# Performance work log

Hardware: AMD Instinct MI355X
Metric: run time of the kernel (lower is better)

Reference implementation:

```python
import jax, jax.numpy as jnp
import numpy as np

B, S, D, H = 2, 2048, 1024, 16
RANK = int(D * 0.2)  # 204, per decom(): rank = int(min(a,b)*ratio_LR)
HEAD = D // H


def setup_inputs() -> dict:
    key = jax.random.key(0)
    ks = jax.random.split(key, 16)
    s_in = 1.0 / np.sqrt(D)
    s_r = 1.0 / np.sqrt(RANK)
    inp = {
        'q': jax.random.normal(ks[0], (B, S, D), jnp.float32),
        'k': jax.random.normal(ks[1], (B, S, D), jnp.float32),
        'v': jax.random.normal(ks[2], (B, S, D), jnp.float32),
    }
    names = ['q', 'k', 'v', 'o']
    for i, n in enumerate(names):
        inp[f'V{n}'] = jax.random.uniform(ks[3 + 3 * i], (RANK, D), jnp.float32, -s_in, s_in)
        inp[f'U{n}'] = jax.random.uniform(ks[4 + 3 * i], (D, RANK), jnp.float32, -s_r, s_r)
        inp[f'b{n}'] = jax.random.uniform(ks[5 + 3 * i], (D,), jnp.float32, -s_r, s_r)
    return inp


def _factorized(x, Vw, Uw, b):
    # x @ V^T @ U^T + b  (low-rank linear: Linear(D->rank, no bias) then Linear(rank->D, bias))
    return jnp.einsum('bsr,dr->bsd', jnp.einsum('bsd,rd->bsr', x, Vw), Uw) + b


def _split_heads(x):
    # [B,S,D] -> [B,H,S,HEAD]
    return x.reshape(B, S, H, HEAD).transpose(0, 2, 1, 3)


def reference(q, k, v, Vq, Uq, bq, Vk, Uk, bk, Vv, Uv, bv, Vo, Uo, bo):
    qh = _split_heads(_factorized(q, Vq, Uq, bq))
    kh = _split_heads(_factorized(k, Vk, Uk, bk))
    vh = _split_heads(_factorized(v, Vv, Uv, bv))
    temperature = jnp.asarray(HEAD, jnp.float32) ** 0.5
    scores = jnp.einsum('bhqd,bhkd->bhqk', qh, kh) / temperature
    causal = jnp.tril(jnp.ones((S, S), bool))  # recreated each call in original
    scores = jnp.where(causal, scores, -jnp.inf)
    attn = jax.nn.softmax(scores, axis=-1)  # [B,H,S,S]
    out = jnp.einsum('bhqk,bhkd->bhqd', attn, vh)
    out = out.transpose(0, 2, 1, 3).reshape(B, S, D)
    out = _factorized(out, Vo, Uo, bo)
    # original returns attn flattened over batch*heads
    return out, attn.reshape(B * H, S, S)
```

## Files before the change

kernel.cpp:

```cpp
#include <hip/hip_runtime.h>
#include <stdint.h>

#define BB   2
#define SS   2048
#define DD   1024
#define NH   16
#define RK   204
#define RKP  256
#define HDIM 64
#define BH   (BB*NH)

typedef __attribute__((ext_vector_type(8))) short short8;
typedef __attribute__((ext_vector_type(4))) float f32x4;
typedef unsigned short u16;
typedef unsigned int   u32;

#define LOG2E  1.4426950408889634f

static __device__ __forceinline__ u32 cvtpk(float lo, float hi) {
    u32 r; asm("v_cvt_pk_bf16_f32 %0, %1, %2" : "=v"(r) : "v"(lo), "v"(hi)); return r;
}
static __device__ __forceinline__ u16 f2bf(float f) { return (u16)cvtpk(f, f); }
static __device__ __forceinline__ u32 pack2(float lo, float hi) { return cvtpk(lo, hi); }
static __device__ __forceinline__ float exp2_hw(float x) {
    float r; asm("v_exp_f32 %0, %1" : "=v"(r) : "v"(x)); return r;
}

struct C4 { const float *s0, *s1, *s2, *s3; u16 *d0, *d1, *d2, *d3; };

__global__ void cvt_bf16_b4(C4 c, int n4) {
    int y = blockIdx.y;
    const float* in = (y==0)?c.s0:(y==1)?c.s1:(y==2)?c.s2:c.s3;
    u16* out = (y==0)?c.d0:(y==1)?c.d1:(y==2)?c.d2:c.d3;
    int i = blockIdx.x * blockDim.x + threadIdx.x;
    if (i < n4) {
        float4 f = ((const float4*)in)[i];
        ((uint2*)out)[i] = make_uint2(pack2(f.x, f.y), pack2(f.z, f.w));
    }
}

__global__ void cvt_pad_b4(C4 c, int n) {
    int y = blockIdx.y;
    const float* in = (y==0)?c.s0:(y==1)?c.s1:(y==2)?c.s2:c.s3;
    u16* out = (y==0)?c.d0:(y==1)?c.d1:(y==2)?c.d2:c.d3;
    int i = blockIdx.x * blockDim.x + threadIdx.x;
    if (i >= n) return;
    int row = i >> 8, col = i & (RKP - 1);
    out[i] = (col < RK) ? f2bf(in[row * RK + col]) : (u16)0;
}

struct B3 {
    const void *A0, *A1, *A2;
    const u16  *B0, *B1, *B2;
    const float *bb0, *bb1, *bb2;
    void *C0, *C1, *C2;
};

#define LDW 136

template<int A_F32, int OUT_F32, int HAS_BIAS, int VT_LAST, int QSC>
__global__ __launch_bounds__(256)
void gemm_nt_k(B3 g, int lda, int ldb, int nrowsB, int ldc, int K)
{
    const int z = blockIdx.z;
    const void* Ap  = (z==0)?g.A0:(z==1)?g.A1:g.A2;
    const u16*  Bp  = (z==0)?g.B0:(z==1)?g.B1:g.B2;
    const float* bias = (z==0)?g.bb0:(z==1)?g.bb1:g.bb2;
    void* Cp = (z==0)?g.C0:(z==1)?g.C1:g.C2;

    __shared__ __align__(16) u16 As[64*LDW];
    __shared__ __align__(16) u16 Bs[64*LDW];
    const int row0 = blockIdx.x * 64;
    const int col0 = blockIdx.y * 64;
    const int t = threadIdx.x;
    const int w = t >> 6, lane = t & 63, quad = lane >> 4, l16 = lane & 15;
    const int r = t >> 2, seg = t & 3;

    f32x4 acc0 = 0.f, acc1 = 0.f, acc2 = 0.f, acc3 = 0.f;

    for (int k0 = 0; k0 < K; k0 += 128) {
        __syncthreads();
        if (A_F32) {
            const float* ga = (const float*)Ap + (size_t)(row0 + r) * lda + k0 + seg*32;
            float4 f0 = ((const float4*)ga)[0];
            float4 f1 = ((const float4*)ga)[1];
            float4 f2 = ((const float4*)ga)[2];
            float4 f3 = ((const float4*)ga)[3];
            float4 f4 = ((const float4*)ga)[4];
            float4 f5 = ((const float4*)ga)[5];
            float4 f6 = ((const float4*)ga)[6];
            float4 f7 = ((const float4*)ga)[7];
            uint4 s0 = { pack2(f0.x,f0.y), pack2(f0.z,f0.w), pack2(f1.x,f1.y), pack2(f1.z,f1.w) };
            uint4 s1 = { pack2(f2.x,f2.y), pack2(f2.z,f2.w), pack2(f3.x,f3.y), pack2(f3.z,f3.w) };
            uint4 s2 = { pack2(f4.x,f4.y), pack2(f4.z,f4.w), pack2(f5.x,f5.y), pack2(f5.z,f5.w) };
            uint4 s3 = { pack2(f6.x,f6.y), pack2(f6.z,f6.w), pack2(f7.x,f7.y), pack2(f7.z,f7.w) };
            *(uint4*)(As + r*LDW + seg*32)      = s0;
            *(uint4*)(As + r*LDW + seg*32 + 8)  = s1;
            *(uint4*)(As + r*LDW + seg*32 + 16) = s2;
            *(uint4*)(As + r*LDW + seg*32 + 24) = s3;
        } else {
            const u16* ga = (const u16*)Ap + (size_t)(row0 + r) * lda + k0 + seg*32;
            *(uint4*)(As + r*LDW + seg*32)      = ((const uint4*)ga)[0];
            *(uint4*)(As + r*LDW + seg*32 + 8)  = ((const uint4*)ga)[1];
            *(uint4*)(As + r*LDW + seg*32 + 16) = ((const uint4*)ga)[2];
            *(uint4*)(As + r*LDW + seg*32 + 24) = ((const uint4*)ga)[3];
        }
        {
            uint4 b0 = {0,0,0,0}, b1 = {0,0,0,0}, b2 = {0,0,0,0}, b3 = {0,0,0,0};
            if (col0 + r < nrowsB) {
                const u16* gb = Bp + (size_t)(col0 + r) * ldb + k0 + seg*32;
                b0 = ((const uint4*)gb)[0];
                b1 = ((const uint4*)gb)[1];
                b2 = ((const uint4*)gb)[2];
                b3 = ((const uint4*)gb)[3];
            }
            *(uint4*)(Bs + r*LDW + seg*32)      = b0;
            *(uint4*)(Bs + r*LDW + seg*32 + 8)  = b1;
            *(uint4*)(Bs + r*LDW + seg*32 + 16) = b2;
            *(uint4*)(Bs + r*LDW + seg*32 + 24) = b3;
        }
        __syncthreads();
        #pragma unroll
        for (int c = 0; c < 4; ++c) {
            short8 a = *(const short8*)(As + (w*16 + l16)*LDW + c*32 + quad*8);
            short8 b0v = *(const short8*)(Bs + (0*16 + l16)*LDW + c*32 + quad*8);
            acc0 = __builtin_amdgcn_mfma_f32_16x16x32_bf16(a, b0v, acc0, 0, 0, 0);
            short8 b1v = *(const short8*)(Bs + (1*16 + l16)*LDW + c*32 + quad*8);
            acc1 = __builtin_amdgcn_mfma_f32_16x16x32_bf16(a, b1v, acc1, 0, 0, 0);
            short8 b2v = *(const short8*)(Bs + (2*16 + l16)*LDW + c*32 + quad*8);
            acc2 = __builtin_amdgcn_mfma_f32_16x16x32_bf16(a, b2v, acc2, 0, 0, 0);
            short8 b3v = *(const short8*)(Bs + (3*16 + l16)*LDW + c*32 + quad*8);
            acc3 = __builtin_amdgcn_mfma_f32_16x16x32_bf16(a, b3v, acc3, 0, 0, 0);
        }
    }

    if (VT_LAST && z == 2) {
        __syncthreads();
        #pragma unroll
        for (int f = 0; f < 4; ++f) {
            f32x4 a = (f==0) ? acc0 : (f==1) ? acc1 : (f==2) ? acc2 : acc3;
            int col = f*16 + l16;
            float bv = HAS_BIAS ? bias[col0 + col] : 0.f;
            #pragma unroll
            for (int rg = 0; rg < 4; ++rg) {
                int rowl = w*16 + quad*4 + rg;
                As[col*72 + rowl] = f2bf(a[rg] + bv);
            }
        }
        __syncthreads();
        const int b_ = row0 >> 11;
        const int s0 = row0 & (SS - 1);
        const int h  = col0 >> 6;
        u16* dst = (u16*)Cp + ((size_t)((b_*NH + h)*HDIM + r))*SS + s0 + seg*16;
        ((uint4*)dst)[0] = *(const uint4*)(As + r*72 + seg*16);
        ((uint4*)dst)[1] = *(const uint4*)(As + r*72 + seg*16 + 8);
        return;
    }

    const float osc = (QSC && z == 0) ? 0.125f : 1.f;
    #pragma unroll
    for (int f = 0; f < 4; ++f) {
        f32x4 a = (f==0) ? acc0 : (f==1) ? acc1 : (f==2) ? acc2 : acc3;
        int col = col0 + f*16 + l16;
        float bv = HAS_BIAS ? bias[col] : 0.f;
        #pragma unroll
        for (int rg = 0; rg < 4; ++rg) {
            int rowg = row0 + w*16 + quad*4 + rg;
            float val = (a[rg] + bv) * osc;
            if (col >= nrowsB) val = 0.f;
            if (OUT_F32) ((float*)Cp)[(size_t)rowg*ldc + col] = val;
            else         ((u16*)Cp)[(size_t)rowg*ldc + col]  = f2bf(val);
        }
    }
}

#define QKT_8(BUF,sa0,sa1,sa2,sa3) do { \
    short8 b0 = *(const short8*)(BUF + (0*16 + l16)*72 + quad*8); \
    sa0 = __builtin_amdgcn_mfma_f32_16x16x32_bf16(q0, b0, sa0, 0,0,0); \
    short8 b0b = *(const short8*)(BUF + (0*16 + l16)*72 + 32 + quad*8); \
    sa0 = __builtin_amdgcn_mfma_f32_16x16x32_bf16(q1, b0b, sa0, 0,0,0); \
    short8 b1 = *(const short8*)(BUF + (1*16 + l16)*72 + quad*8); \
    sa1 = __builtin_amdgcn_mfma_f32_16x16x32_bf16(q0, b1, sa1, 0,0,0); \
    short8 b1b = *(const short8*)(BUF + (1*16 + l16)*72 + 32 + quad*8); \
    sa1 = __builtin_amdgcn_mfma_f32_16x16x32_bf16(q1, b1b, sa1, 0,0,0); \
    short8 b2 = *(const short8*)(BUF + (2*16 + l16)*72 + quad*8); \
    sa2 = __builtin_amdgcn_mfma_f32_16x16x32_bf16(q0, b2, sa2, 0,0,0); \
    short8 b2b = *(const short8*)(BUF + (2*16 + l16)*72 + 32 + quad*8); \
    sa2 = __builtin_amdgcn_mfma_f32_16x16x32_bf16(q1, b2b, sa2, 0,0,0); \
    short8 b3 = *(const short8*)(BUF + (3*16 + l16)*72 + quad*8); \
    sa3 = __builtin_amdgcn_mfma_f32_16x16x32_bf16(q0, b3, sa3, 0,0,0); \
    short8 b3b = *(const short8*)(BUF + (3*16 + l16)*72 + 32 + quad*8); \
    sa3 = __builtin_amdgcn_mfma_f32_16x16x32_bf16(q1, b3b, sa3, 0,0,0); \
} while (0)

static __device__ __forceinline__ void p1_int(
    const f32x4& sa0, const f32x4& sa1, const f32x4& sa2, const f32x4& sa3, float* l)
{
    #pragma unroll
    for (int rg = 0; rg < 4; ++rg) {
        l[rg] += (exp2_hw(sa0[rg]*LOG2E) + exp2_hw(sa1[rg]*LOG2E))
               + (exp2_hw(sa2[rg]*LOG2E) + exp2_hw(sa3[rg]*LOG2E));
    }
}
static __device__ __forceinline__ void p1_diag(
    const f32x4& sa0, const f32x4& sa1, const f32x4& sa2, const f32x4& sa3,
    float* l, int key0, int qg0)
{
    #pragma unroll
    for (int rg = 0; rg < 4; ++rg) {
        int qg = qg0 + rg;
        float e0 = (key0      <= qg) ? exp2_hw(sa0[rg]*LOG2E) : 0.f;
        float e1 = (key0 + 16 <= qg) ? exp2_hw(sa1[rg]*LOG2E) : 0.f;
        float e2 = (key0 + 32 <= qg) ? exp2_hw(sa2[rg]*LOG2E) : 0.f;
        float e3 = (key0 + 48 <= qg) ? exp2_hw(sa3[rg]*LOG2E) : 0.f;
        l[rg] += (e0+e1) + (e2+e3);
    }
}

__global__ __launch_bounds__(256)
void attn_k(const u16* __restrict__ qh, const u16* __restrict__ kh,
            const u16* __restrict__ vT,
            float* __restrict__ attn_out, u16* __restrict__ Ob)
{
    __shared__ __align__(16) u16 Ks[64*72];
    __shared__ __align__(16) u16 Vs[64*72];
    __shared__ __align__(16) u16 Ps[64*72];
    const int blk = blockIdx.x;
    const int qt = blk & 31, bh = blk >> 5;
    const int b_ = bh >> 4, h = bh & (NH - 1);
    const int qbase = qt * 64;
    const int t = threadIdx.x, w = t >> 6, lane = t & 63, quad = lane >> 4, l16 = lane & 15;
    const int r = t >> 2, seg = t & 3;

    const u16* qrow = qh + (size_t)(b_*SS + qbase + w*16 + l16)*DD + h*HDIM;
    short8 q0 = *(const short8*)(qrow + quad*8);
    short8 q1 = *(const short8*)(qrow + 32 + quad*8);

    const u16* kstage = kh + (size_t)(b_*SS + r)*DD + h*HDIM + seg*16;
    const u16* vstage = vT + ((size_t)(bh*HDIM + r))*SS + seg*16;
    const int qg0 = qbase + w*16 + quad*4;

    float l[4] = {0.f, 0.f, 0.f, 0.f};

    for (int kt0 = 0; kt0 <= qt; kt0 += 2) {
        const bool two = (kt0 + 1) <= qt;
        __syncthreads();
        {
            const u16* krow = kstage + (size_t)kt0*64*DD;
            *(uint4*)(Ks + r*72 + seg*16)     = ((const uint4*)krow)[0];
            *(uint4*)(Ks + r*72 + seg*16 + 8) = ((const uint4*)krow)[1];
            if (two) {
                const u16* krow2 = krow + (size_t)64*DD;
                *(uint4*)(Vs + r*72 + seg*16)     = ((const uint4*)krow2)[0];
                *(uint4*)(Vs + r*72 + seg*16 + 8) = ((const uint4*)krow2)[1];
            }
        }
        __syncthreads();
        {
            f32x4 sa0 = 0.f, sa1 = 0.f, sa2 = 0.f, sa3 = 0.f;
            QKT_8(Ks, sa0, sa1, sa2, sa3);
            if (kt0 < qt) p1_int(sa0, sa1, sa2, sa3, l);
            else          p1_diag(sa0, sa1, sa2, sa3, l, kt0*64 + l16, qg0);
        }
        if (two) {
            f32x4 sa0 = 0.f, sa1 = 0.f, sa2 = 0.f, sa3 = 0.f;
            QKT_8(Vs, sa0, sa1, sa2, sa3);
            if (kt0 + 1 < qt) p1_int(sa0, sa1, sa2, sa3, l);
            else              p1_diag(sa0, sa1, sa2, sa3, l, (kt0+1)*64 + l16, qg0);
        }
    }

    float lg2rl[4];
    #pragma unroll
    for (int rg = 0; rg < 4; ++rg) {
        #pragma unroll
        for (int d = 1; d < 16; d <<= 1) l[rg] += __shfl_xor(l[rg], d);
        lg2rl[rg] = -__log2f(l[rg]);
    }

    f32x4 oa0 = 0.f, oa1 = 0.f, oa2 = 0.f, oa3 = 0.f;
    float* attn_base = attn_out + (size_t)bh * SS * SS;
    float* rp0 = attn_base + (size_t)(qg0 + 0)*SS + l16;
    float* rp1 = attn_base + (size_t)(qg0 + 1)*SS + l16;
    float* rp2 = attn_base + (size_t)(qg0 + 2)*SS + l16;
    float* rp3 = attn_base + (size_t)(qg0 + 3)*SS + l16;
    const int psrow = w*16 + quad*4;

    for (int kt = 0; kt <= qt; ++kt) {
        __syncthreads();
        {
            const u16* krow = kstage + (size_t)kt*64*DD;
            *(uint4*)(Ks + r*72 + seg*16)     = ((const uint4*)krow)[0];
            *(uint4*)(Ks + r*72 + seg*16 + 8) = ((const uint4*)krow)[1];
            const u16* vrow = vstage + kt*64;
            *(uint4*)(Vs + r*72 + seg*16)     = ((const uint4*)vrow)[0];
            *(uint4*)(Vs + r*72 + seg*16 + 8) = ((const uint4*)vrow)[1];
        }
        __syncthreads();

        f32x4 sa0 = 0.f, sa1 = 0.f, sa2 = 0.f, sa3 = 0.f;
        QKT_8(Ks, sa0, sa1, sa2, sa3);

        if (kt < qt) {
            #pragma unroll
            for (int f = 0; f < 4; ++f) {
                f32x4 sv = (f==0) ? sa0 : (f==1) ? sa1 : (f==2) ? sa2 : sa3;
                float p0 = exp2_hw(__builtin_fmaf(sv[0], LOG2E, lg2rl[0]));
                float p1 = exp2_hw(__builtin_fmaf(sv[1], LOG2E, lg2rl[1]));
                float p2 = exp2_hw(__builtin_fmaf(sv[2], LOG2E, lg2rl[2]));
                float p3 = exp2_hw(__builtin_fmaf(sv[3], LOG2E, lg2rl[3]));
                rp0[f*16] = p0; rp1[f*16] = p1; rp2[f*16] = p2; rp3[f*16] = p3;
                u32 pk01 = cvtpk(p0, p1), pk23 = cvtpk(p2, p3);
                Ps[(psrow+0)*72 + f*16 + l16] = (u16)pk01;
                Ps[(psrow+1)*72 + f*16 + l16] = (u16)(pk01 >> 16);
                Ps[(psrow+2)*72 + f*16 + l16] = (u16)pk23;
                Ps[(psrow+3)*72 + f*16 + l16] = (u16)(pk23 >> 16);
            }
        } else {
            int kbase = kt*64;
            #pragma unroll
            for (int f = 0; f < 4; ++f) {
                f32x4 sv = (f==0) ? sa0 : (f==1) ? sa1 : (f==2) ? sa2 : sa3;
                int key = kbase + f*16 + l16;
                float p0 = (key <= qg0+0) ? exp2_hw(__builtin_fmaf(sv[0], LOG2E, lg2rl[0])) : 0.f;
                float p1 = (key <= qg0+1) ? exp2_hw(__builtin_fmaf(sv[1], LOG2E, lg2rl[1])) : 0.f;
                float p2 = (key <= qg0+2) ? exp2_hw(__builtin_fmaf(sv[2], LOG2E, lg2rl[2])) : 0.f;
                float p3 = (key <= qg0+3) ? exp2_hw(__builtin_fmaf(sv[3], LOG2E, lg2rl[3])) : 0.f;
                rp0[f*16] = p0; rp1[f*16] = p1; rp2[f*16] = p2; rp3[f*16] = p3;
                u32 pk01 = cvtpk(p0, p1), pk23 = cvtpk(p2, p3);
                Ps[(psrow+0)*72 + f*16 + l16] = (u16)pk01;
                Ps[(psrow+1)*72 + f*16 + l16] = (u16)(pk01 >> 16);
                Ps[(psrow+2)*72 + f*16 + l16] = (u16)pk23;
                Ps[(psrow+3)*72 + f*16 + l16] = (u16)(pk23 >> 16);
            }
        }
        rp0 += 64; rp1 += 64; rp2 += 64; rp3 += 64;

        asm volatile("" ::: "memory");

        #pragma unroll
        for (int c = 0; c < 2; ++c) {
            short8 pa = *(const short8*)(Ps + (w*16 + l16)*72 + c*32 + quad*8);
            short8 v0 = *(const short8*)(Vs + (0*16 + l16)*72 + c*32 + quad*8);
            oa0 = __builtin_amdgcn_mfma_f32_16x16x32_bf16(pa, v0, oa0, 0,0,0);
            short8 v1 = *(const short8*)(Vs + (1*16 + l16)*72 + c*32 + quad*8);
            oa1 = __builtin_amdgcn_mfma_f32_16x16x32_bf16(pa, v1, oa1, 0,0,0);
            short8 v2 = *(const short8*)(Vs + (2*16 + l16)*72 + c*32 + quad*8);
            oa2 = __builtin_amdgcn_mfma_f32_16x16x32_bf16(pa, v2, oa2, 0,0,0);
            short8 v3 = *(const short8*)(Vs + (3*16 + l16)*72 + c*32 + quad*8);
            oa3 = __builtin_amdgcn_mfma_f32_16x16x32_bf16(pa, v3, oa3, 0,0,0);
        }
    }

    for (int kt = qt + 1; kt < 32; ++kt) {
        int kbase = kt * 64;
        f32x4 z = 0.f;
        f32x4* p = (f32x4*)(attn_base + (size_t)(qbase + r)*SS + kbase + seg*16);
        p[0] = z; p[1] = z; p[2] = z; p[3] = z;
    }

    #pragma unroll
    for (int f = 0; f < 4; ++f) {
        f32x4 ov = (f==0) ? oa0 : (f==1) ? oa1 : (f==2) ? oa2 : oa3;
        #pragma unroll
        for (int rg = 0; rg < 4; ++rg) {
            int qg = qg0 + rg;
            Ob[(size_t)(b_*SS + qg)*DD + h*HDIM + f*16 + l16] = f2bf(ov[rg]);
        }
    }
}

extern "C" void kernel_launch(void* const* d_in, const int* in_sizes, int n_in,
                              void* d_out, int out_size, void* d_ws, size_t ws_size,
                              hipStream_t stream)
{
    const float* xs[3] = { (const float*)d_in[0], (const float*)d_in[1], (const float*)d_in[2] };
    const float* Vw[4] = { (const float*)d_in[3], (const float*)d_in[6], (const float*)d_in[9],  (const float*)d_in[12] };
    const float* Uw[4] = { (const float*)d_in[4], (const float*)d_in[7], (const float*)d_in[10], (const float*)d_in[13] };
    const float* bw[4] = { (const float*)d_in[5], (const float*)d_in[8], (const float*)d_in[11], (const float*)d_in[14] };

    char* ws = (char*)d_ws;
    size_t off = 0;
    auto alloc = [&](size_t bytes) -> char* {
        char* p = ws + off;
        off += (bytes + 255) & ~(size_t)255;
        return p;
    };
    u16* wV[4]; for (int i = 0; i < 4; ++i) wV[i] = (u16*)alloc((size_t)RK*DD*2);
    u16* wU[4]; for (int i = 0; i < 4; ++i) wU[i] = (u16*)alloc((size_t)DD*RKP*2);
    u16* Tb[3]; for (int i = 0; i < 3; ++i) Tb[i] = (u16*)alloc((size_t)BB*SS*RKP*2);
    u16* hb[2]; for (int i = 0; i < 2; ++i) hb[i] = (u16*)alloc((size_t)BB*SS*DD*2);
    u16* vTb = (u16*)alloc((size_t)BB*SS*DD*2);
    u16* Ob  = (u16*)alloc((size_t)BB*SS*DD*2);
    (void)ws_size; (void)in_sizes; (void)n_in; (void)out_size;

    {
        C4 cv = { Vw[0], Vw[1], Vw[2], Vw[3], wV[0], wV[1], wV[2], wV[3] };
        cvt_bf16_b4<<<dim3((RK*DD/4 + 255)/256, 4), 256, 0, stream>>>(cv, RK*DD/4);
        C4 cu = { Uw[0], Uw[1], Uw[2], Uw[3], wU[0], wU[1], wU[2], wU[3] };
        cvt_pad_b4<<<dim3((DD*RKP + 255)/256, 4), 256, 0, stream>>>(cu, DD*RKP);
    }

    const int MROWS = BB*SS;
    {
        B3 g = { xs[0], xs[1], xs[2], wV[0], wV[1], wV[2],
                 nullptr, nullptr, nullptr, Tb[0], Tb[1], Tb[2] };
        gemm_nt_k<1,0,0,0,0><<<dim3(MROWS/64, RKP/64, 3), 256, 0, stream>>>(
            g, DD, DD, RK, RKP, DD);
    }
    {
        B3 g = { Tb[0], Tb[1], Tb[2], wU[0], wU[1], wU[2],
                 bw[0], bw[1], bw[2], hb[0], hb[1], vTb };
        gemm_nt_k<0,0,1,1,1><<<dim3(MROWS/64, DD/64, 3), 256, 0, stream>>>(
            g, RKP, RKP, DD, DD, RKP);
    }

    float* attn_out = (float*)d_out + (size_t)BB*SS*DD;
    attn_k<<<BH*32, 256, 0, stream>>>(hb[0], hb[1], vTb, attn_out, Ob);

    {
        B3 g = { Ob, Ob, Ob, wV[3], wV[3], wV[3],
                 nullptr, nullptr, nullptr, Tb[0], Tb[0], Tb[0] };
        gemm_nt_k<0,0,0,0,0><<<dim3(MROWS/64, RKP/64, 1), 256, 0, stream>>>(
            g, DD, DD, RK, RKP, DD);
    }
    {
        B3 g = { Tb[0], Tb[0], Tb[0], wU[3], wU[3], wU[3],
                 bw[3], bw[3], bw[3], d_out, d_out, d_out };
        gemm_nt_k<0,1,1,0,0><<<dim3(MROWS/64, DD/64, 1), 256, 0, stream>>>(
            g, RKP, RKP, DD, DD, RKP);
    }
}
```

Measured before the change: 747.5 us.

## Double attention query tile to 128 rows with 512 threads, merge weight conversions

The attention kernel now processes 128 query rows per block with 8 waves, so each staged K/V tile is shared by twice as many queries. This halves the K/V global loads per query and the number of blocks. The two weight-conversion kernels are merged into one launch. The bigger tiles cut grid parallelism, and for the diagonal region the causal imbalance becomes coarser, since a block now covers two diagonal tiles.

```diff
diff --git a/kernel.cpp b/kernel.cpp
--- a/kernel.cpp
+++ b/kernel.cpp
@@ -26,27 +26,22 @@
     float r; asm("v_exp_f32 %0, %1" : "=v"(r) : "v"(x)); return r;
 }
 
-struct C4 { const float *s0, *s1, *s2, *s3; u16 *d0, *d1, *d2, *d3; };
-
-__global__ void cvt_bf16_b4(C4 c, int n4) {
+struct C8 { const float* s[8]; u16* d[8]; };
+
+__global__ void cvt_all_k(C8 c) {
     int y = blockIdx.y;
-    const float* in = (y==0)?c.s0:(y==1)?c.s1:(y==2)?c.s2:c.s3;
-    u16* out = (y==0)?c.d0:(y==1)?c.d1:(y==2)?c.d2:c.d3;
     int i = blockIdx.x * blockDim.x + threadIdx.x;
-    if (i < n4) {
-        float4 f = ((const float4*)in)[i];
-        ((uint2*)out)[i] = make_uint2(pack2(f.x, f.y), pack2(f.z, f.w));
-    }
-}
-
-__global__ void cvt_pad_b4(C4 c, int n) {
-    int y = blockIdx.y;
-    const float* in = (y==0)?c.s0:(y==1)?c.s1:(y==2)?c.s2:c.s3;
-    u16* out = (y==0)?c.d0:(y==1)?c.d1:(y==2)?c.d2:c.d3;
-    int i = blockIdx.x * blockDim.x + threadIdx.x;
-    if (i >= n) return;
-    int row = i >> 8, col = i & (RKP - 1);
-    out[i] = (col < RK) ? f2bf(in[row * RK + col]) : (u16)0;
+    if (y < 4) {
+        if (i < RK*DD/4) {
+            float4 f = ((const float4*)c.s[y])[i];
+            ((uint2*)c.d[y])[i] = make_uint2(pack2(f.x, f.y), pack2(f.z, f.w));
+        }
+    } else {
+        if (i < DD*RKP) {
+            int row = i >> 8, col = i & (RKP - 1);
+            c.d[y][i] = (col < RK) ? f2bf(c.s[y][row * RK + col]) : (u16)0;
+        }
+    }
 }
 
 struct B3 {
@@ -217,56 +212,52 @@
     }
 }
 
-__global__ __launch_bounds__(256)
+__global__ __launch_bounds__(512)
 void attn_k(const u16* __restrict__ qh, const u16* __restrict__ kh,
             const u16* __restrict__ vT,
             float* __restrict__ attn_out, u16* __restrict__ Ob)
 {
     __shared__ __align__(16) u16 Ks[64*72];
     __shared__ __align__(16) u16 Vs[64*72];
-    __shared__ __align__(16) u16 Ps[64*72];
+    __shared__ __align__(16) u16 Ps[128*72];
     const int blk = blockIdx.x;
-    const int qt = blk & 31, bh = blk >> 5;
+    const int i_ = blk & 15, bh = blk >> 4;
     const int b_ = bh >> 4, h = bh & (NH - 1);
-    const int qbase = qt * 64;
+    const int qbase = i_ * 128;
+    const int qtTop = 2*i_ + 1;
     const int t = threadIdx.x, w = t >> 6, lane = t & 63, quad = lane >> 4, l16 = lane & 15;
-    const int r = t >> 2, seg = t & 3;
+    const int rs = t >> 3, seg8 = t & 7;
+    const int r2 = t >> 2, seg = t & 3;
 
     const u16* qrow = qh + (size_t)(b_*SS + qbase + w*16 + l16)*DD + h*HDIM;
     short8 q0 = *(const short8*)(qrow + quad*8);
     short8 q1 = *(const short8*)(qrow + 32 + quad*8);
 
-    const u16* kstage = kh + (size_t)(b_*SS + r)*DD + h*HDIM + seg*16;
-    const u16* vstage = vT + ((size_t)(bh*HDIM + r))*SS + seg*16;
+    const u16* kstage = kh + (size_t)(b_*SS + rs)*DD + h*HDIM + seg8*8;
+    const u16* vstage = vT + ((size_t)(bh*HDIM + rs))*SS + seg8*8;
     const int qg0 = qbase + w*16 + quad*4;
 
     float l[4] = {0.f, 0.f, 0.f, 0.f};
 
-    for (int kt0 = 0; kt0 <= qt; kt0 += 2) {
-        const bool two = (kt0 + 1) <= qt;
+    for (int kt0 = 0; kt0 <= qtTop; kt0 += 2) {
         __syncthreads();
         {
             const u16* krow = kstage + (size_t)kt0*64*DD;
-            *(uint4*)(Ks + r*72 + seg*16)     = ((const uint4*)krow)[0];
-            *(uint4*)(Ks + r*72 + seg*16 + 8) = ((const uint4*)krow)[1];
-            if (two) {
-                const u16* krow2 = krow + (size_t)64*DD;
-                *(uint4*)(Vs + r*72 + seg*16)     = ((const uint4*)krow2)[0];
-                *(uint4*)(Vs + r*72 + seg*16 + 8) = ((const uint4*)krow2)[1];
-            }
+            *(uint4*)(Ks + rs*72 + seg8*8) = *(const uint4*)krow;
+            *(uint4*)(Vs + rs*72 + seg8*8) = *(const uint4*)(krow + (size_t)64*DD);
         }
         __syncthreads();
         {
             f32x4 sa0 = 0.f, sa1 = 0.f, sa2 = 0.f, sa3 = 0.f;
             QKT_8(Ks, sa0, sa1, sa2, sa3);
-            if (kt0 < qt) p1_int(sa0, sa1, sa2, sa3, l);
-            else          p1_diag(sa0, sa1, sa2, sa3, l, kt0*64 + l16, qg0);
-        }
-        if (two) {
+            if (kt0 < 2*i_) p1_int(sa0, sa1, sa2, sa3, l);
+            else            p1_diag(sa0, sa1, sa2, sa3, l, kt0*64 + l16, qg0);
+        }
+        {
             f32x4 sa0 = 0.f, sa1 = 0.f, sa2 = 0.f, sa3 = 0.f;
             QKT_8(Vs, sa0, sa1, sa2, sa3);
-            if (kt0 + 1 < qt) p1_int(sa0, sa1, sa2, sa3, l);
-            else              p1_diag(sa0, sa1, sa2, sa3, l, (kt0+1)*64 + l16, qg0);
+            if (kt0 < 2*i_) p1_int(sa0, sa1, sa2, sa3, l);
+            else            p1_diag(sa0, sa1, sa2, sa3, l, (kt0+1)*64 + l16, qg0);
         }
     }
 
@@ -286,22 +277,20 @@
     float* rp3 = attn_base + (size_t)(qg0 + 3)*SS + l16;
     const int psrow = w*16 + quad*4;
 
-    for (int kt = 0; kt <= qt; ++kt) {
+    for (int kt = 0; kt <= qtTop; ++kt) {
         __syncthreads();
         {
             const u16* krow = kstage + (size_t)kt*64*DD;
-            *(uint4*)(Ks + r*72 + seg*16)     = ((const uint4*)krow)[0];
-            *(uint4*)(Ks + r*72 + seg*16 + 8) = ((const uint4*)krow)[1];
+            *(uint4*)(Ks + rs*72 + seg8*8) = *(const uint4*)krow;
             const u16* vrow = vstage + kt*64;
-            *(uint4*)(Vs + r*72 + seg*16)     = ((const uint4*)vrow)[0];
-            *(uint4*)(Vs + r*72 + seg*16 + 8) = ((const uint4*)vrow)[1];
+            *(uint4*)(Vs + rs*72 + seg8*8) = *(const uint4*)vrow;
         }
         __syncthreads();
 
         f32x4 sa0 = 0.f, sa1 = 0.f, sa2 = 0.f, sa3 = 0.f;
         QKT_8(Ks, sa0, sa1, sa2, sa3);
 
-        if (kt < qt) {
+        if (kt < 2*i_) {
             #pragma unroll
             for (int f = 0; f < 4; ++f) {
                 f32x4 sv = (f==0) ? sa0 : (f==1) ? sa1 : (f==2) ? sa2 : sa3;
@@ -352,10 +341,10 @@
         }
     }
 
-    for (int kt = qt + 1; kt < 32; ++kt) {
+    for (int kt = qtTop + 1; kt < 32; ++kt) {
         int kbase = kt * 64;
         f32x4 z = 0.f;
-        f32x4* p = (f32x4*)(attn_base + (size_t)(qbase + r)*SS + kbase + seg*16);
+        f32x4* p = (f32x4*)(attn_base + (size_t)(qbase + r2)*SS + kbase + seg*16);
         p[0] = z; p[1] = z; p[2] = z; p[3] = z;
     }
 
@@ -395,10 +384,9 @@
     (void)ws_size; (void)in_sizes; (void)n_in; (void)out_size;
 
     {
-        C4 cv = { Vw[0], Vw[1], Vw[2], Vw[3], wV[0], wV[1], wV[2], wV[3] };
-        cvt_bf16_b4<<<dim3((RK*DD/4 + 255)/256, 4), 256, 0, stream>>>(cv, RK*DD/4);
-        C4 cu = { Uw[0], Uw[1], Uw[2], Uw[3], wU[0], wU[1], wU[2], wU[3] };
-        cvt_pad_b4<<<dim3((DD*RKP + 255)/256, 4), 256, 0, stream>>>(cu, DD*RKP);
+        C8 c = { { Vw[0], Vw[1], Vw[2], Vw[3], Uw[0], Uw[1], Uw[2], Uw[3] },
+                 { wV[0], wV[1], wV[2], wV[3], wU[0], wU[1], wU[2], wU[3] } };
+        cvt_all_k<<<dim3((DD*RKP + 255)/256, 8), 256, 0, stream>>>(c);
     }
 
     const int MROWS = BB*SS;
@@ -416,7 +404,7 @@
     }
 
     float* attn_out = (float*)d_out + (size_t)BB*SS*DD;
-    attn_k<<<BH*32, 256, 0, stream>>>(hb[0], hb[1], vTb, attn_out, Ob);
+    attn_k<<<BH*16, 512, 0, stream>>>(hb[0], hb[1], vTb, attn_out, Ob);
 
     {
         B3 g = { Ob, Ob, Ob, wV[3], wV[3], wV[3],
```

Measured after the change: 737.3 us. About the same (-1.4%).
